# Optimization experiments

Measured on AMD Instinct MI355X. Metric: run time of the kernel, lower is better.

Reference implementation:

```python
import jax, jax.numpy as jnp
import numpy as np

B, T, C, H = 2, 2048, 1024, 16
D = C // H  # head_dim = 64


def setup_inputs() -> dict:
    key = jax.random.key(0)
    ks = jax.random.split(key, 12)
    s = 1.0 / np.sqrt(C)
    inp = {
        "q": jax.random.normal(ks[0], (B, T, C), jnp.float32),
        "k": jax.random.normal(ks[1], (B, T, C), jnp.float32),
        "v": jax.random.normal(ks[2], (B, T, C), jnp.float32),
        "mask": jnp.tril(jnp.ones((T, T), jnp.int32)),  # causal mask; 0 = masked
        "Wq": jax.random.normal(ks[3], (C, C), jnp.float32) * s,
        "bq": jax.random.normal(ks[4], (C,), jnp.float32) * s,
        "Wk": jax.random.normal(ks[5], (C, C), jnp.float32) * s,
        "bk": jax.random.normal(ks[6], (C,), jnp.float32) * s,
        "Wv": jax.random.normal(ks[7], (C, C), jnp.float32) * s,
        "bv": jax.random.normal(ks[8], (C,), jnp.float32) * s,
        "Wo": jax.random.normal(ks[9], (C, C), jnp.float32) * s,
        "bo": jax.random.normal(ks[10], (C,), jnp.float32) * s,
    }
    return inp


def reference(q, k, v, mask, Wq, bq, Wk, bk, Wv, bv, Wo, bo):
    # Linear projections (torch Linear: x @ W.T + b)
    qh = (q @ Wq.T + bq).reshape(B, T, H, D).transpose(0, 2, 1, 3)  # [B,H,T,D]
    kh = (k @ Wk.T + bk).reshape(B, -1, H, D).transpose(0, 2, 1, 3)
    vh = (v @ Wv.T + bv).reshape(B, -1, H, D).transpose(0, 2, 1, 3)
    scores = jnp.einsum("bhtd,bhsd->bhts", qh, kh) / jnp.sqrt(jnp.float32(D))
    scores = jnp.where(mask[None, None, :, :] == 0, -jnp.inf, scores)
    attn = jax.nn.softmax(scores, axis=-1)
    out = jnp.einsum("bhts,bhsd->bhtd", attn, vh)  # [B,H,T,D]
    out = out.transpose(0, 2, 1, 3).reshape(B, T, C)
    return out @ Wo.T + bo
```

## Files before the change

kernel.cpp:

```cpp
#include <hip/hip_runtime.h>
#include <hip/hip_bf16.h>

#define BB 2
#define TT 2048
#define CC 1024
#define HH 16
#define DD 64
#define MM (BB * TT)

typedef __bf16 bf16;
typedef __bf16 bf16x4 __attribute__((ext_vector_type(4)));
typedef __bf16 bf16x8 __attribute__((ext_vector_type(8)));
typedef float f32x4 __attribute__((ext_vector_type(4)));

__device__ __forceinline__ void gload16(const bf16* g, bf16* l) {
    __builtin_amdgcn_global_load_lds(
        (__attribute__((address_space(1))) void*)g,
        (__attribute__((address_space(3))) void*)l, 16, 0, 0);
}

__global__ __launch_bounds__(256) void to_bf16(
    const float* __restrict__ q, const float* __restrict__ k,
    const float* __restrict__ v,
    const float* __restrict__ wq, const float* __restrict__ wk,
    const float* __restrict__ wv, const float* __restrict__ wo,
    bf16* __restrict__ xq, bf16* __restrict__ xk, bf16* __restrict__ xv,
    bf16* __restrict__ owq, bf16* __restrict__ owk, bf16* __restrict__ owv,
    bf16* __restrict__ owo)
{
    const unsigned XE = 1u << 22;
    const unsigned WE = 1u << 20;
    const unsigned NC = (3u * XE + 4u * WE) >> 3;
    for (unsigned c = blockIdx.x * blockDim.x + threadIdx.x; c < NC;
         c += gridDim.x * blockDim.x) {
        const unsigned e = c << 3;
        const float* src; bf16* dst; unsigned off;
        if (e < 3u * XE) {
            const unsigned t = e >> 22; off = e & (XE - 1u);
            src = (t == 0) ? q : (t == 1) ? k : v;
            dst = (t == 0) ? xq : (t == 1) ? xk : xv;
        } else {
            const unsigned e2 = e - 3u * XE;
            const unsigned t = e2 >> 20; off = e2 & (WE - 1u);
            src = (t == 0) ? wq : (t == 1) ? wk : (t == 2) ? wv : wo;
            dst = (t == 0) ? owq : (t == 1) ? owk : (t == 2) ? owv : owo;
        }
        const f32x4 a = *reinterpret_cast<const f32x4*>(src + off);
        const f32x4 b = *reinterpret_cast<const f32x4*>(src + off + 4);
        bf16x8 r;
#pragma unroll
        for (int j = 0; j < 4; ++j) { r[j] = (bf16)a[j]; r[j + 4] = (bf16)b[j]; }
        *reinterpret_cast<bf16x8*>(dst + off) = r;
    }
}

template <typename TOUT, int HEAD_LAYOUT>
__device__ __forceinline__ void gemm_tile_body(
    const bf16* __restrict__ X, const bf16* __restrict__ W,
    const float* __restrict__ bias, TOUT* __restrict__ out,
    bf16* lA, bf16* lB, int vmode)
{
    const int tid  = threadIdx.x;
    const int lane = tid & 63;
    const int quad = lane >> 4;
    const int lm   = lane & 15;
    const int wave = tid >> 6;
    const int m0 = blockIdx.x << 7;
    const int n0 = blockIdx.y << 7;
    const int wrow = (wave >> 1) << 6;
    const int wcol = (wave & 1) << 6;

    const int c0 = tid, c1 = tid + 256;
    const bf16* gA0 = X + (size_t)(m0 + (c0 >> 2)) * CC + (c0 & 3) * 8;
    const bf16* gA1 = X + (size_t)(m0 + (c1 >> 2)) * CC + (c1 & 3) * 8;
    const bf16* gB0 = W + (size_t)(n0 + (c0 >> 2)) * CC + (c0 & 3) * 8;
    const bf16* gB1 = W + (size_t)(n0 + (c1 >> 2)) * CC + (c1 & 3) * 8;
    bf16* lAw0 = lA + wave * 512;
    bf16* lAw1 = lA + 2048 + wave * 512;
    bf16* lBw0 = lB + wave * 512;
    bf16* lBw1 = lB + 2048 + wave * 512;

    f32x4 acc[4][4];
#pragma unroll
    for (int i = 0; i < 4; ++i)
#pragma unroll
        for (int j = 0; j < 4; ++j) acc[i][j] = (f32x4){0.f, 0.f, 0.f, 0.f};

    for (int kk = 0; kk < CC; kk += 32) {
        __syncthreads();
        gload16(gA0 + kk, lAw0);
        gload16(gA1 + kk, lAw1);
        gload16(gB0 + kk, lBw0);
        gload16(gB1 + kk, lBw1);
        __syncthreads();

        bf16x8 af[4], bf_[4];
#pragma unroll
        for (int i = 0; i < 4; ++i)
            af[i] = *reinterpret_cast<const bf16x8*>(
                lA + (wrow + i * 16 + lm) * 32 + quad * 8);
#pragma unroll
        for (int j = 0; j < 4; ++j)
            bf_[j] = *reinterpret_cast<const bf16x8*>(
                lB + (wcol + j * 16 + lm) * 32 + quad * 8);
#pragma unroll
        for (int i = 0; i < 4; ++i)
#pragma unroll
            for (int j = 0; j < 4; ++j)
                acc[i][j] = __builtin_amdgcn_mfma_f32_16x16x32_bf16(
                    af[i], bf_[j], acc[i][j], 0, 0, 0);
    }

#pragma unroll
    for (int j = 0; j < 4; ++j) {
        const int col = n0 + wcol + j * 16 + lm;
        const float bv = bias[col];
        if (vmode) {
            const int h = col / DD, d = col % DD;
#pragma unroll
            for (int i = 0; i < 4; ++i) {
                const int m = m0 + wrow + i * 16 + quad * 4;
                const int b_ = m / TT, t = m % TT;
                bf16x4 o;
#pragma unroll
                for (int r = 0; r < 4; ++r) o[r] = (bf16)(acc[i][j][r] + bv);
                *reinterpret_cast<bf16x4*>(
                    (bf16*)out + (((size_t)(b_ * HH + h)) * DD + d) * TT + t) = o;
            }
        } else {
#pragma unroll
            for (int i = 0; i < 4; ++i)
#pragma unroll
                for (int r = 0; r < 4; ++r) {
                    const int m = m0 + wrow + i * 16 + quad * 4 + r;
                    const float v = acc[i][j][r] + bv;
                    if (HEAD_LAYOUT) {
                        const int b_ = m / TT, t = m % TT;
                        const int h = col / DD, d = col % DD;
                        out[(((size_t)(b_ * HH + h)) * TT + t) * DD + d] = (TOUT)v;
                    } else {
                        out[(size_t)m * CC + col] = (TOUT)v;
                    }
                }
        }
    }
}

__global__ __launch_bounds__(256) void gemm_qkv(
    const bf16* __restrict__ x0, const bf16* __restrict__ x1,
    const bf16* __restrict__ x2,
    const bf16* __restrict__ w0, const bf16* __restrict__ w1,
    const bf16* __restrict__ w2,
    const float* __restrict__ b0, const float* __restrict__ b1,
    const float* __restrict__ b2,
    bf16* __restrict__ o0, bf16* __restrict__ o1, bf16* __restrict__ o2)
{
    __shared__ __align__(16) bf16 lA[128 * 32];
    __shared__ __align__(16) bf16 lB[128 * 32];
    const int z = blockIdx.z;
    const bf16* X = (z == 0) ? x0 : (z == 1) ? x1 : x2;
    const bf16* W = (z == 0) ? w0 : (z == 1) ? w1 : w2;
    const float* bias = (z == 0) ? b0 : (z == 1) ? b1 : b2;
    bf16* out = (z == 0) ? o0 : (z == 1) ? o1 : o2;
    gemm_tile_body<bf16, 1>(X, W, bias, out, lA, lB, (z == 2) ? 1 : 0);
}

__global__ __launch_bounds__(256) void gemm_oproj(
    const bf16* __restrict__ X, const bf16* __restrict__ W,
    const float* __restrict__ bias, float* __restrict__ out)
{
    __shared__ __align__(16) bf16 lA[128 * 32];
    __shared__ __align__(16) bf16 lB[128 * 32];
    gemm_tile_body<float, 0>(X, W, bias, out, lA, lB, 0);
}

__global__ __launch_bounds__(256) void attn_fused(
    const bf16* __restrict__ Qh, const bf16* __restrict__ Kh,
    const bf16* __restrict__ Vt, bf16* __restrict__ attn_out)
{
    __shared__ __align__(16) bf16 ldsK[2][64 * 72];
    __shared__ __align__(16) bf16 ldsV[2][16 * 64 * 4];

    const int tid  = threadIdx.x;
    const int lane = tid & 63;
    const int wave = tid >> 6;
    const int xp = blockIdx.x;
    const int bh = blockIdx.y;
    const int b_ = bh >> 4, h = bh & 15;
    const size_t baseQK = (size_t)bh * TT * DD;
    const size_t baseVT = (size_t)bh * DD * TT;
    const int lm   = lane & 15;
    const int quad = lane >> 4;
    const int koff = quad * 8;

    const int kKey = tid >> 3, kDc = tid & 7;
    const int vD   = tid >> 2, vSc = tid & 3;

    for (int pass = 0; pass < 2; ++pass) {
        const int qb = pass == 0 ? (TT / 64 - 1 - xp) : xp;
        const int q0 = qb * 64 + wave * 16;
        const int q_lane = q0 + lm;

        const bf16* qp = Qh + baseQK + (size_t)q_lane * DD + koff;
        bf16x8 qr0 = *reinterpret_cast<const bf16x8*>(qp);
        bf16x8 qr1 = *reinterpret_cast<const bf16x8*>(qp + 32);
        bf16x8 qf0, qf1;
#pragma unroll
        for (int j = 0; j < 8; ++j) {
            qf0[j] = (bf16)((float)qr0[j] * 0.125f);
            qf1[j] = (bf16)((float)qr1[j] * 0.125f);
        }

        f32x4 Oacc[4];
#pragma unroll
        for (int dt = 0; dt < 4; ++dt) Oacc[dt] = (f32x4){0.f, 0.f, 0.f, 0.f};
        float m_run = -1e30f, l_run = 0.f;

        bf16x8 kreg[2], vreg[2];
#pragma unroll
        for (int it = 0; it < 2; ++it) {
            kreg[it] = *reinterpret_cast<const bf16x8*>(
                Kh + baseQK + (size_t)(kKey + it * 32) * DD + kDc * 8);
            vreg[it] = *reinterpret_cast<const bf16x8*>(
                Vt + baseVT + (size_t)vD * TT + (vSc + it * 4) * 8);
        }
        __syncthreads();

        for (int kb = 0; kb <= qb; ++kb) {
            const int cur = kb & 1;

#pragma unroll
            for (int it = 0; it < 2; ++it) {
                const int key = kKey + it * 32;
                *reinterpret_cast<bf16x8*>(
                    &ldsK[cur][key * 72 + kDc * 8]) = kreg[it];
                const int sc = vSc + it * 4;
                bf16x4 lo, hi;
#pragma unroll
                for (int j = 0; j < 4; ++j) {
                    lo[j] = vreg[it][j]; hi[j] = vreg[it][4 + j];
                }
                *reinterpret_cast<bf16x4*>(
                    &ldsV[cur][((2 * sc) * 64 + vD) * 4]) = lo;
                *reinterpret_cast<bf16x4*>(
                    &ldsV[cur][((2 * sc + 1) * 64 + vD) * 4]) = hi;
            }
            __syncthreads();

            if (kb < qb) {
                const int s0n = (kb + 1) * 64;
#pragma unroll
                for (int it = 0; it < 2; ++it) {
                    kreg[it] = *reinterpret_cast<const bf16x8*>(
                        Kh + baseQK + (size_t)(s0n + kKey + it * 32) * DD
                        + kDc * 8);
                    vreg[it] = *reinterpret_cast<const bf16x8*>(
                        Vt + baseVT + (size_t)vD * TT + s0n
                        + (vSc + it * 4) * 8);
                }
            }

            float sv[4][4];
            __builtin_amdgcn_s_setprio(1);
#pragma unroll
            for (int st = 0; st < 4; ++st) {
                const bf16* kp = &ldsK[cur][(st * 16 + lm) * 72 + koff];
                bf16x8 k0 = *reinterpret_cast<const bf16x8*>(kp);
                bf16x8 k1 = *reinterpret_cast<const bf16x8*>(kp + 32);
                f32x4 s = {0.f, 0.f, 0.f, 0.f};
                s = __builtin_amdgcn_mfma_f32_16x16x32_bf16(k0, qf0, s, 0, 0, 0);
                s = __builtin_amdgcn_mfma_f32_16x16x32_bf16(k1, qf1, s, 0, 0, 0);
#pragma unroll
                for (int r = 0; r < 4; ++r) sv[st][r] = s[r];
            }
            __builtin_amdgcn_s_setprio(0);

            if (kb == qb) {
                const int s0 = kb * 64;
#pragma unroll
                for (int st = 0; st < 4; ++st) {
                    const int kbase = s0 + st * 16 + quad * 4;
#pragma unroll
                    for (int r = 0; r < 4; ++r)
                        if (kbase + r > q_lane) sv[st][r] = -1e30f;
                }
            }

            float mx = sv[0][0];
#pragma unroll
            for (int st = 0; st < 4; ++st)
#pragma unroll
                for (int r = 0; r < 4; ++r) mx = fmaxf(mx, sv[st][r]);
            mx = fmaxf(mx, __shfl_xor(mx, 16));
            mx = fmaxf(mx, __shfl_xor(mx, 32));
            if (__any(mx > m_run)) {
                const float mn = fmaxf(m_run, mx);
                const float alpha = __expf(m_run - mn);
                m_run = mn;
                l_run *= alpha;
#pragma unroll
                for (int dt = 0; dt < 4; ++dt) Oacc[dt] *= alpha;
            }
            float srow = 0.f;
#pragma unroll
            for (int st = 0; st < 4; ++st)
#pragma unroll
                for (int r = 0; r < 4; ++r) {
                    const float p = __expf(sv[st][r] - m_run);
                    sv[st][r] = p;
                    srow += p;
                }
            srow += __shfl_xor(srow, 16);
            srow += __shfl_xor(srow, 32);
            l_run += srow;

            bf16x8 pf[2];
#pragma unroll
            for (int c = 0; c < 2; ++c)
#pragma unroll
                for (int j = 0; j < 4; ++j) {
                    pf[c][j]     = (bf16)sv[2 * c][j];
                    pf[c][4 + j] = (bf16)sv[2 * c + 1][j];
                }

            __builtin_amdgcn_s_setprio(1);
#pragma unroll
            for (int dt = 0; dt < 4; ++dt) {
                const int d = dt * 16 + lm;
#pragma unroll
                for (int c = 0; c < 2; ++c) {
                    bf16x4 v0 = *reinterpret_cast<const bf16x4*>(
                        &ldsV[cur][((c * 8 + quad) * 64 + d) * 4]);
                    bf16x4 v1 = *reinterpret_cast<const bf16x4*>(
                        &ldsV[cur][((c * 8 + 4 + quad) * 64 + d) * 4]);
                    bf16x8 vf;
#pragma unroll
                    for (int j = 0; j < 4; ++j) { vf[j] = v0[j]; vf[4 + j] = v1[j]; }
                    Oacc[dt] = __builtin_amdgcn_mfma_f32_16x16x32_bf16(
                        vf, pf[c], Oacc[dt], 0, 0, 0);
                }
            }
            __builtin_amdgcn_s_setprio(0);
        }

        const float inv_l = 1.0f / l_run;
        bf16* dst = attn_out + ((size_t)(b_ * TT + q_lane)) * CC + h * DD;
#pragma unroll
        for (int dt = 0; dt < 4; ++dt) {
            bf16x4 o;
#pragma unroll
            for (int r = 0; r < 4; ++r) o[r] = (bf16)(Oacc[dt][r] * inv_l);
            *reinterpret_cast<bf16x4*>(dst + dt * 16 + quad * 4) = o;
        }
    }
}

extern "C" void kernel_launch(void* const* d_in, const int* in_sizes, int n_in,
                              void* d_out, int out_size, void* d_ws,
                              size_t ws_size, hipStream_t stream)
{
    const float* q  = (const float*)d_in[0];
    const float* k  = (const float*)d_in[1];
    const float* v  = (const float*)d_in[2];
    const float* Wq = (const float*)d_in[4];
    const float* bq = (const float*)d_in[5];
    const float* Wk = (const float*)d_in[6];
    const float* bk = (const float*)d_in[7];
    const float* Wv = (const float*)d_in[8];
    const float* bv = (const float*)d_in[9];
    const float* Wo = (const float*)d_in[10];
    const float* bo = (const float*)d_in[11];
    float* out = (float*)d_out;

    bf16* Qh   = (bf16*)d_ws;
    bf16* Kh   = Qh + (size_t)MM * CC;
    bf16* Vt   = Kh + (size_t)MM * CC;
    bf16* attn = Vt + (size_t)MM * CC;
    bf16* Xq   = attn + (size_t)MM * CC;
    bf16* Xk   = Xq + (size_t)MM * CC;
    bf16* Xv   = Xk + (size_t)MM * CC;
    bf16* Wqb  = Xv + (size_t)MM * CC;
    bf16* Wkb  = Wqb + (size_t)CC * CC;
    bf16* Wvb  = Wkb + (size_t)CC * CC;
    bf16* Wob  = Wvb + (size_t)CC * CC;

    const dim3 blk(256);
    to_bf16<<<dim3(2048), blk, 0, stream>>>(
        q, k, v, Wq, Wk, Wv, Wo, Xq, Xk, Xv, Wqb, Wkb, Wvb, Wob);
    gemm_qkv<<<dim3(MM / 128, CC / 128, 3), blk, 0, stream>>>(
        Xq, Xk, Xv, Wqb, Wkb, Wvb, bq, bk, bv, Qh, Kh, Vt);
    attn_fused<<<dim3(TT / 128, BB * HH), blk, 0, stream>>>(Qh, Kh, Vt, attn);
    gemm_oproj<<<dim3(MM / 128, CC / 128), blk, 0, stream>>>(
        attn, Wob, bo, out);
}
```

Before: 234.7 us.

## Process key tiles in pairs with quad-buffered LDS and repacked V layout

The attention loop now handles two 64-key tiles per iteration. It uses four LDS buffers and prefetches the next two tiles into registers, so there are half as many barriers and online-softmax rescales per key. The V tile is stored in LDS so each MFMA operand is one 16-byte read instead of two 8-byte reads plus a shuffle. The costs are higher register pressure from the doubled score and prefetch registers, double the LDS footprint, and a separate tail path for an odd tile count.

Result: faster. 227.6 us (-3.0%).

```diff
diff --git a/kernel.cpp b/kernel.cpp
--- a/kernel.cpp
+++ b/kernel.cpp
@@ -174,12 +174,69 @@
     gemm_tile_body<float, 0>(X, W, bias, out, lA, lB, 0);
 }
 
+__device__ __forceinline__ void issue_k(const bf16* __restrict__ Kh,
+                                        size_t baseQK, int s0, int kKey,
+                                        int kDc, bf16x8* kreg) {
+#pragma unroll
+    for (int it = 0; it < 2; ++it)
+        kreg[it] = *reinterpret_cast<const bf16x8*>(
+            Kh + baseQK + (size_t)(s0 + kKey + it * 32) * DD + kDc * 8);
+}
+__device__ __forceinline__ void issue_v(const bf16* __restrict__ Vt,
+                                        size_t baseVT, int s0, int vD,
+                                        int vSc, bf16x8* vreg) {
+#pragma unroll
+    for (int it = 0; it < 2; ++it)
+        vreg[it] = *reinterpret_cast<const bf16x8*>(
+            Vt + baseVT + (size_t)vD * TT + s0 + (vSc + it * 4) * 8);
+}
+__device__ __forceinline__ void write_k(bf16* buf, int kKey, int kDc,
+                                        const bf16x8* kreg) {
+#pragma unroll
+    for (int it = 0; it < 2; ++it)
+        *reinterpret_cast<bf16x8*>(&buf[(kKey + it * 32) * 72 + kDc * 8]) =
+            kreg[it];
+}
+__device__ __forceinline__ void write_v(bf16* buf, int vD, int vSc,
+                                        const bf16x8* vreg) {
+#pragma unroll
+    for (int it = 0; it < 2; ++it) {
+        const int sc = vSc + it * 4;
+        const int c2 = sc >> 2, h = (sc >> 1) & 1, q0 = (sc & 1) * 2;
+        bf16x4 lo, hi;
+#pragma unroll
+        for (int j = 0; j < 4; ++j) { lo[j] = vreg[it][j]; hi[j] = vreg[it][4 + j]; }
+        *reinterpret_cast<bf16x4*>(
+            &buf[((c2 * 4 + q0) * 64 + vD) * 8 + h * 4]) = lo;
+        *reinterpret_cast<bf16x4*>(
+            &buf[((c2 * 4 + q0 + 1) * 64 + vD) * 8 + h * 4]) = hi;
+    }
+}
+__device__ __forceinline__ void qk_tile(const bf16* bufK, int lm, int koff,
+                                        bf16x8 qf0, bf16x8 qf1,
+                                        float sv[4][4]) {
+#pragma unroll
+    for (int st = 0; st < 4; ++st) {
+        const bf16* kp = &bufK[(st * 16 + lm) * 72 + koff];
+        bf16x8 k0 = *reinterpret_cast<const bf16x8*>(kp);
+        bf16x8 k1 = *reinterpret_cast<const bf16x8*>(kp + 32);
+        f32x4 s = {0.f, 0.f, 0.f, 0.f};
+        s = __builtin_amdgcn_mfma_f32_16x16x32_bf16(k0, qf0, s, 0, 0, 0);
+        s = __builtin_amdgcn_mfma_f32_16x16x32_bf16(k1, qf1, s, 0, 0, 0);
+#pragma unroll
+        for (int r = 0; r < 4; ++r) sv[st][r] = s[r];
+    }
+}
+__device__ __forceinline__ float tmax4(const float s[4]) {
+    return fmaxf(fmaxf(s[0], s[1]), fmaxf(s[2], s[3]));
+}
+
 __global__ __launch_bounds__(256) void attn_fused(
     const bf16* __restrict__ Qh, const bf16* __restrict__ Kh,
     const bf16* __restrict__ Vt, bf16* __restrict__ attn_out)
 {
-    __shared__ __align__(16) bf16 ldsK[2][64 * 72];
-    __shared__ __align__(16) bf16 ldsV[2][16 * 64 * 4];
+    __shared__ __align__(16) bf16 ldsK[4][64 * 72];
+    __shared__ __align__(16) bf16 ldsV[4][8 * 64 * 8];
 
     const int tid  = threadIdx.x;
     const int lane = tid & 63;
@@ -200,6 +257,9 @@
         const int qb = pass == 0 ? (TT / 64 - 1 - xp) : xp;
         const int q0 = qb * 64 + wave * 16;
         const int q_lane = q0 + lm;
+        const int ntiles = qb + 1;
+        const int npairs = ntiles >> 1;
+        const int has_tail = ntiles & 1;
 
         const bf16* qp = Qh + baseQK + (size_t)q_lane * DD + koff;
         bf16x8 qr0 = *reinterpret_cast<const bf16x8*>(qp);
@@ -216,81 +276,57 @@
         for (int dt = 0; dt < 4; ++dt) Oacc[dt] = (f32x4){0.f, 0.f, 0.f, 0.f};
         float m_run = -1e30f, l_run = 0.f;
 
-        bf16x8 kreg[2], vreg[2];
-#pragma unroll
-        for (int it = 0; it < 2; ++it) {
-            kreg[it] = *reinterpret_cast<const bf16x8*>(
-                Kh + baseQK + (size_t)(kKey + it * 32) * DD + kDc * 8);
-            vreg[it] = *reinterpret_cast<const bf16x8*>(
-                Vt + baseVT + (size_t)vD * TT + (vSc + it * 4) * 8);
+        bf16x8 kregA[2], vregA[2], kregB[2], vregB[2];
+        issue_k(Kh, baseQK, 0, kKey, kDc, kregA);
+        issue_v(Vt, baseVT, 0, vD, vSc, vregA);
+        if (ntiles > 1) {
+            issue_k(Kh, baseQK, 64, kKey, kDc, kregB);
+            issue_v(Vt, baseVT, 64, vD, vSc, vregB);
         }
         __syncthreads();
 
-        for (int kb = 0; kb <= qb; ++kb) {
-            const int cur = kb & 1;
-
-#pragma unroll
-            for (int it = 0; it < 2; ++it) {
-                const int key = kKey + it * 32;
-                *reinterpret_cast<bf16x8*>(
-                    &ldsK[cur][key * 72 + kDc * 8]) = kreg[it];
-                const int sc = vSc + it * 4;
-                bf16x4 lo, hi;
-#pragma unroll
-                for (int j = 0; j < 4; ++j) {
-                    lo[j] = vreg[it][j]; hi[j] = vreg[it][4 + j];
+        int base = 0;
+        for (int j = 0; j < npairs; ++j) {
+            const int t1 = 2 * j + 1;
+
+            write_k(ldsK[base], kKey, kDc, kregA);
+            write_v(ldsV[base], vD, vSc, vregA);
+            write_k(ldsK[base + 1], kKey, kDc, kregB);
+            write_v(ldsV[base + 1], vD, vSc, vregB);
+            __syncthreads();
+
+            if (t1 + 1 < ntiles) {
+                issue_k(Kh, baseQK, (t1 + 1) * 64, kKey, kDc, kregA);
+                issue_v(Vt, baseVT, (t1 + 1) * 64, vD, vSc, vregA);
+            }
+            if (t1 + 2 < ntiles) {
+                issue_k(Kh, baseQK, (t1 + 2) * 64, kKey, kDc, kregB);
+                issue_v(Vt, baseVT, (t1 + 2) * 64, vD, vSc, vregB);
+            }
+
+            float svA[4][4], svB[4][4];
+            __builtin_amdgcn_s_setprio(1);
+            qk_tile(ldsK[base], lm, koff, qf0, qf1, svA);
+            qk_tile(ldsK[base + 1], lm, koff, qf0, qf1, svB);
+            __builtin_amdgcn_s_setprio(0);
+
+            if (t1 == qb) {
+                const int s0b = t1 * 64;
+#pragma unroll
+                for (int st = 0; st < 4; ++st) {
+                    const int kbase = s0b + st * 16 + quad * 4;
+#pragma unroll
+                    for (int r = 0; r < 4; ++r)
+                        if (kbase + r > q_lane) svB[st][r] = -1e30f;
                 }
-                *reinterpret_cast<bf16x4*>(
-                    &ldsV[cur][((2 * sc) * 64 + vD) * 4]) = lo;
-                *reinterpret_cast<bf16x4*>(
-                    &ldsV[cur][((2 * sc + 1) * 64 + vD) * 4]) = hi;
-            }
-            __syncthreads();
-
-            if (kb < qb) {
-                const int s0n = (kb + 1) * 64;
-#pragma unroll
-                for (int it = 0; it < 2; ++it) {
-                    kreg[it] = *reinterpret_cast<const bf16x8*>(
-                        Kh + baseQK + (size_t)(s0n + kKey + it * 32) * DD
-                        + kDc * 8);
-                    vreg[it] = *reinterpret_cast<const bf16x8*>(
-                        Vt + baseVT + (size_t)vD * TT + s0n
-                        + (vSc + it * 4) * 8);
-                }
-            }
-
-            float sv[4][4];
-            __builtin_amdgcn_s_setprio(1);
-#pragma unroll
-            for (int st = 0; st < 4; ++st) {
-                const bf16* kp = &ldsK[cur][(st * 16 + lm) * 72 + koff];
-                bf16x8 k0 = *reinterpret_cast<const bf16x8*>(kp);
-                bf16x8 k1 = *reinterpret_cast<const bf16x8*>(kp + 32);
-                f32x4 s = {0.f, 0.f, 0.f, 0.f};
-                s = __builtin_amdgcn_mfma_f32_16x16x32_bf16(k0, qf0, s, 0, 0, 0);
-                s = __builtin_amdgcn_mfma_f32_16x16x32_bf16(k1, qf1, s, 0, 0, 0);
-#pragma unroll
-                for (int r = 0; r < 4; ++r) sv[st][r] = s[r];
-            }
-            __builtin_amdgcn_s_setprio(0);
-
-            if (kb == qb) {
-                const int s0 = kb * 64;
-#pragma unroll
-                for (int st = 0; st < 4; ++st) {
-                    const int kbase = s0 + st * 16 + quad * 4;
-#pragma unroll
-                    for (int r = 0; r < 4; ++r)
-                        if (kbase + r > q_lane) sv[st][r] = -1e30f;
-                }
-            }
-
-            float mx = sv[0][0];
-#pragma unroll
-            for (int st = 0; st < 4; ++st)
-#pragma unroll
-                for (int r = 0; r < 4; ++r) mx = fmaxf(mx, sv[st][r]);
+            }
+
+            float rm[8];
+#pragma unroll
+            for (int st = 0; st < 4; ++st) { rm[st] = tmax4(svA[st]); rm[4 + st] = tmax4(svB[st]); }
+            float mx = fmaxf(
+                fmaxf(fmaxf(rm[0], rm[1]), fmaxf(rm[2], rm[3])),
+                fmaxf(fmaxf(rm[4], rm[5]), fmaxf(rm[6], rm[7])));
             mx = fmaxf(mx, __shfl_xor(mx, 16));
             mx = fmaxf(mx, __shfl_xor(mx, 32));
             if (__any(mx > m_run)) {
@@ -301,26 +337,37 @@
 #pragma unroll
                 for (int dt = 0; dt < 4; ++dt) Oacc[dt] *= alpha;
             }
-            float srow = 0.f;
-#pragma unroll
-            for (int st = 0; st < 4; ++st)
-#pragma unroll
-                for (int r = 0; r < 4; ++r) {
-                    const float p = __expf(sv[st][r] - m_run);
-                    sv[st][r] = p;
-                    srow += p;
-                }
+            float ps[8];
+#pragma unroll
+            for (int st = 0; st < 4; ++st) {
+                float p0 = __expf(svA[st][0] - m_run);
+                float p1 = __expf(svA[st][1] - m_run);
+                float p2 = __expf(svA[st][2] - m_run);
+                float p3 = __expf(svA[st][3] - m_run);
+                svA[st][0] = p0; svA[st][1] = p1; svA[st][2] = p2; svA[st][3] = p3;
+                ps[st] = (p0 + p1) + (p2 + p3);
+                float b0 = __expf(svB[st][0] - m_run);
+                float b1 = __expf(svB[st][1] - m_run);
+                float b2 = __expf(svB[st][2] - m_run);
+                float b3 = __expf(svB[st][3] - m_run);
+                svB[st][0] = b0; svB[st][1] = b1; svB[st][2] = b2; svB[st][3] = b3;
+                ps[4 + st] = (b0 + b1) + (b2 + b3);
+            }
+            float srow = ((ps[0] + ps[1]) + (ps[2] + ps[3]))
+                       + ((ps[4] + ps[5]) + (ps[6] + ps[7]));
             srow += __shfl_xor(srow, 16);
             srow += __shfl_xor(srow, 32);
             l_run += srow;
 
-            bf16x8 pf[2];
+            bf16x8 pf[4];
 #pragma unroll
             for (int c = 0; c < 2; ++c)
 #pragma unroll
-                for (int j = 0; j < 4; ++j) {
-                    pf[c][j]     = (bf16)sv[2 * c][j];
-                    pf[c][4 + j] = (bf16)sv[2 * c + 1][j];
+                for (int jj = 0; jj < 4; ++jj) {
+                    pf[c][jj]         = (bf16)svA[2 * c][jj];
+                    pf[c][4 + jj]     = (bf16)svA[2 * c + 1][jj];
+                    pf[2 + c][jj]     = (bf16)svB[2 * c][jj];
+                    pf[2 + c][4 + jj] = (bf16)svB[2 * c + 1][jj];
                 }
 
             __builtin_amdgcn_s_setprio(1);
@@ -328,14 +375,80 @@
             for (int dt = 0; dt < 4; ++dt) {
                 const int d = dt * 16 + lm;
 #pragma unroll
+                for (int c = 0; c < 4; ++c) {
+                    const bf16* vp = &ldsV[base + (c >> 1)]
+                        [(((c & 1) * 4 + quad) * 64 + d) * 8];
+                    bf16x8 vf = *reinterpret_cast<const bf16x8*>(vp);
+                    Oacc[dt] = __builtin_amdgcn_mfma_f32_16x16x32_bf16(
+                        vf, pf[c], Oacc[dt], 0, 0, 0);
+                }
+            }
+            __builtin_amdgcn_s_setprio(0);
+            base ^= 2;
+        }
+
+        if (has_tail) {
+            write_k(ldsK[base], kKey, kDc, kregA);
+            write_v(ldsV[base], vD, vSc, vregA);
+            __syncthreads();
+
+            float sv[4][4];
+            __builtin_amdgcn_s_setprio(1);
+            qk_tile(ldsK[base], lm, koff, qf0, qf1, sv);
+            __builtin_amdgcn_s_setprio(0);
+            const int s0 = qb * 64;
+#pragma unroll
+            for (int st = 0; st < 4; ++st) {
+                const int kbase = s0 + st * 16 + quad * 4;
+#pragma unroll
+                for (int r = 0; r < 4; ++r)
+                    if (kbase + r > q_lane) sv[st][r] = -1e30f;
+            }
+            float rm[4];
+#pragma unroll
+            for (int st = 0; st < 4; ++st) rm[st] = tmax4(sv[st]);
+            float mx = fmaxf(fmaxf(rm[0], rm[1]), fmaxf(rm[2], rm[3]));
+            mx = fmaxf(mx, __shfl_xor(mx, 16));
+            mx = fmaxf(mx, __shfl_xor(mx, 32));
+            if (__any(mx > m_run)) {
+                const float mn = fmaxf(m_run, mx);
+                const float alpha = __expf(m_run - mn);
+                m_run = mn;
+                l_run *= alpha;
+#pragma unroll
+                for (int dt = 0; dt < 4; ++dt) Oacc[dt] *= alpha;
+            }
+            float ps[4];
+#pragma unroll
+            for (int st = 0; st < 4; ++st) {
+                float p0 = __expf(sv[st][0] - m_run);
+                float p1 = __expf(sv[st][1] - m_run);
+                float p2 = __expf(sv[st][2] - m_run);
+                float p3 = __expf(sv[st][3] - m_run);
+                sv[st][0] = p0; sv[st][1] = p1; sv[st][2] = p2; sv[st][3] = p3;
+                ps[st] = (p0 + p1) + (p2 + p3);
+            }
+            float srow = (ps[0] + ps[1]) + (ps[2] + ps[3]);
+            srow += __shfl_xor(srow, 16);
+            srow += __shfl_xor(srow, 32);
+            l_run += srow;
+
+            bf16x8 pf[2];
+#pragma unroll
+            for (int c = 0; c < 2; ++c)
+#pragma unroll
+                for (int jj = 0; jj < 4; ++jj) {
+                    pf[c][jj]     = (bf16)sv[2 * c][jj];
+                    pf[c][4 + jj] = (bf16)sv[2 * c + 1][jj];
+                }
+            __builtin_amdgcn_s_setprio(1);
+#pragma unroll
+            for (int dt = 0; dt < 4; ++dt) {
+                const int d = dt * 16 + lm;
+#pragma unroll
                 for (int c = 0; c < 2; ++c) {
-                    bf16x4 v0 = *reinterpret_cast<const bf16x4*>(
-                        &ldsV[cur][((c * 8 + quad) * 64 + d) * 4]);
-                    bf16x4 v1 = *reinterpret_cast<const bf16x4*>(
-                        &ldsV[cur][((c * 8 + 4 + quad) * 64 + d) * 4]);
-                    bf16x8 vf;
-#pragma unroll
-                    for (int j = 0; j < 4; ++j) { vf[j] = v0[j]; vf[4 + j] = v1[j]; }
+                    const bf16* vp = &ldsV[base][((c * 4 + quad) * 64 + d) * 8];
+                    bf16x8 vf = *reinterpret_cast<const bf16x8*>(vp);
                     Oacc[dt] = __builtin_amdgcn_mfma_f32_16x16x32_bf16(
                         vf, pf[c], Oacc[dt], 0, 0, 0);
                 }
```
